# Kernel tuning notes

Measured on AMD Instinct MI355X. Metric: run time of the kernel, lower is better.

The kernel has to match this reference:

```python
import jax, jax.numpy as jnp
import numpy as np


def setup_inputs() -> dict:
    key = jax.random.key(0)
    ks = jax.random.split(key, 5)
    B, S, D = 2, 2048, 1024
    inv = 1.0 / np.sqrt(D)
    inp = {
        "x": jax.random.normal(ks[0], (B, S, D), jnp.float32),
        "Wq": jax.random.normal(ks[1], (D, D), jnp.float32) * inv,
        "bq": jnp.zeros((D,), jnp.float32),
        "Wk": jax.random.normal(ks[2], (D, D), jnp.float32) * inv,
        "bk": jnp.zeros((D,), jnp.float32),
        "Wv": jax.random.normal(ks[3], (D, D), jnp.float32) * inv,
        "bv": jnp.zeros((D,), jnp.float32),
        "Wo": jax.random.normal(ks[4], (D, D), jnp.float32) * inv,
        "bo": jnp.zeros((D,), jnp.float32),
        "num_heads": 16,
        "window_size": 128,
    }
    return inp


def reference(x, Wq, bq, Wk, bk, Wv, bv, Wo, bo, num_heads, window_size):
    B, S, D = x.shape
    H = num_heads
    hd = D // H
    scale = 1.0 / np.sqrt(hd)

    def split_heads(t):  # [B,S,D] -> [B,H,S,hd]
        return t.reshape(B, S, H, hd).transpose(0, 2, 1, 3)

    q = split_heads(x @ Wq + bq)
    k = split_heads(x @ Wk + bk)
    v = split_heads(x @ Wv + bv)

    # dense scores, then sliding-window + causal mask (faithful to original)
    scores = jnp.einsum('bhqd,bhkd->bhqk', q, k) * scale  # [B,H,S,S]
    i = jnp.arange(S)[:, None]
    j = jnp.arange(S)[None, :]
    # position i attends to j in [i - window_size + 1, i]
    mask = (j <= i) & (j > i - window_size)
    scores = jnp.where(mask, scores, -jnp.inf)
    attn_weights = jax.nn.softmax(scores, axis=-1)  # dropout is identity in eval

    out = jnp.einsum('bhqk,bhkd->bhqd', attn_weights, v)  # [B,H,S,hd]
    out = out.transpose(0, 2, 1, 3).reshape(B, S, D)
    return out @ Wo + bo, attn_weights
```

## Files before the change

### kernel.cpp

```cpp
#include <hip/hip_runtime.h>
#include <cmath>

typedef __attribute__((ext_vector_type(8))) __bf16 v8bf;
typedef __attribute__((ext_vector_type(4))) float  v4f;

#define DEV static __device__ __forceinline__

DEV unsigned short f2bf(float f) {
  unsigned u = __builtin_bit_cast(unsigned, f);
  unsigned r = u + 0x7fffu + ((u >> 16) & 1u);
  return (unsigned short)(r >> 16);
}
DEV float bf2f(unsigned short s) {
  return __builtin_bit_cast(float, ((unsigned)s) << 16);
}
DEV v8bf ld8(const unsigned short* p) { return *(const v8bf*)p; }

DEV void gl16(const unsigned short* g, unsigned short* l) {
  __builtin_amdgcn_global_load_lds(
      (const __attribute__((address_space(1))) unsigned int*)g,
      (__attribute__((address_space(3))) unsigned int*)l, 16, 0, 0);
}

DEV void zero_rows(float* __restrict__ wout, int rbase, int wave, int lane) {
  int r0 = rbase + wave * 4;
  for (int rr = 0; rr < 4; rr++) {
    int row = r0 + rr;
    int i = row & 2047;
    int lo = i - 127;
    float* rowp = wout + (size_t)row * 2048;
#pragma unroll
    for (int it = 0; it < 8; it++) {
      int col = it * 256 + lane * 4;
      bool full_in = (col >= lo) && (col + 3 <= i);
      if (full_in) continue;
      bool overlap = (col + 3 >= lo) && (col <= i);
      if (!overlap) {
        v4f z = {0.f, 0.f, 0.f, 0.f};
        __builtin_nontemporal_store(z, (v4f*)(rowp + col));
      } else {
#pragma unroll
        for (int e = 0; e < 4; e++) {
          int j = col + e;
          if (j < lo || j > i) rowp[j] = 0.f;
        }
      }
    }
  }
}

__global__ __launch_bounds__(256) void k_prep(const float* __restrict__ x,
                                              const float* __restrict__ Wq,
                                              const float* __restrict__ Wk,
                                              const float* __restrict__ Wv,
                                              const float* __restrict__ Wo,
                                              const float* __restrict__ bq,
                                              const float* __restrict__ bk,
                                              const float* __restrict__ bv,
                                              unsigned short* __restrict__ xb,
                                              unsigned short* __restrict__ WT,
                                              unsigned short* __restrict__ WoT,
                                              float* __restrict__ bqkv) {
  __shared__ float t[32][33];
  int bx = blockIdx.x, tid = threadIdx.x;
  if (bx < 4096) {
    int i = bx * 256 + tid;
    float4 v = ((const float4*)x)[i];
    unsigned lo = (unsigned)f2bf(v.x) | ((unsigned)f2bf(v.y) << 16);
    unsigned hi = (unsigned)f2bf(v.z) | ((unsigned)f2bf(v.w) << 16);
    ((uint2*)xb)[i] = make_uint2(lo, hi);
  } else if (bx < 8192) {
    int rem = bx - 4096;
    int z = rem >> 10, r2 = rem & 1023;
    const float* src = (z == 0) ? Wq : (z == 1) ? Wk : (z == 2) ? Wv : Wo;
    unsigned short* dst = (z < 3) ? WT + z * 1048576 : WoT;
    int n0 = (r2 & 31) * 32, k0 = (r2 >> 5) * 32;
    int tx = tid & 31, ty = tid >> 5;
    for (int r = ty; r < 32; r += 8)
      t[r][tx] = src[(k0 + r) * 1024 + n0 + tx];
    __syncthreads();
    for (int r = ty; r < 32; r += 8)
      dst[(n0 + r) * 1024 + k0 + tx] = f2bf(t[tx][r]);
  } else {
    int i = (bx - 8192) * 256 + tid;
    float v = (i < 1024) ? bq[i] : (i < 2048 ? bk[i - 1024] : bv[i - 2048]);
    bqkv[i] = v;
  }
}

__global__ __launch_bounds__(256) void k_gemm1(const unsigned short* __restrict__ A,
                                               const unsigned short* __restrict__ Bt,
                                               const float* __restrict__ bias,
                                               unsigned short* __restrict__ QK,
                                               unsigned short* __restrict__ Vtg) {
  constexpr int K = 1024;
  __shared__ __attribute__((aligned(16))) unsigned short As[128 * 32];
  __shared__ __attribute__((aligned(16))) unsigned short Bs[128 * 32];
  int tid = threadIdx.x;
  int wave = tid >> 6, lane = tid & 63;
  int gid = blockIdx.x;
  int n0 = (gid % 24) * 128, m0 = (gid / 24) * 128;
  int wm = (wave >> 1) * 64, wn = (wave & 1) * 64;
  int m = lane & 15, q4 = lane >> 4;
  int arow = tid >> 2, acol = (tid & 3) * 8;
  v4f acc[4][4] = {};
  const unsigned short* ga0 = A + (m0 + arow) * K + acol;
  const unsigned short* ga1 = A + (m0 + 64 + arow) * K + acol;
  const unsigned short* gb0 = Bt + (n0 + arow) * K + acol;
  const unsigned short* gb1 = Bt + (n0 + 64 + arow) * K + acol;
  unsigned short* lA0 = As + wave * 512;
  unsigned short* lA1 = As + 2048 + wave * 512;
  unsigned short* lB0 = Bs + wave * 512;
  unsigned short* lB1 = Bs + 2048 + wave * 512;

  for (int kt = 0; kt < K; kt += 32) {
    gl16(ga0 + kt, lA0);
    gl16(ga1 + kt, lA1);
    gl16(gb0 + kt, lB0);
    gl16(gb1 + kt, lB1);
    __syncthreads();
    v8bf af[4], bfv[4];
#pragma unroll
    for (int mt = 0; mt < 4; mt++) af[mt] = ld8(&As[(wm + mt * 16 + m) * 32 + q4 * 8]);
#pragma unroll
    for (int nt = 0; nt < 4; nt++) bfv[nt] = ld8(&Bs[(wn + nt * 16 + m) * 32 + q4 * 8]);
#pragma unroll
    for (int mt = 0; mt < 4; mt++)
#pragma unroll
      for (int nt = 0; nt < 4; nt++)
        acc[mt][nt] = __builtin_amdgcn_mfma_f32_16x16x32_bf16(af[mt], bfv[nt], acc[mt][nt], 0, 0, 0);
    __syncthreads();
  }
  if (n0 < 2048) {
#pragma unroll
    for (int mt = 0; mt < 4; mt++)
#pragma unroll
      for (int nt = 0; nt < 4; nt++) {
        int col = n0 + wn + nt * 16 + m;
        float bb = bias[col];
#pragma unroll
        for (int r = 0; r < 4; r++) {
          int row = m0 + wm + mt * 16 + q4 * 4 + r;
          QK[row * 2048 + col] = f2bf(acc[mt][nt][r] + bb);
        }
      }
  } else {
    int b = m0 >> 11;
#pragma unroll
    for (int mt = 0; mt < 4; mt++)
#pragma unroll
      for (int nt = 0; nt < 4; nt++) {
        int d = n0 - 2048 + wn + nt * 16 + m;
        int h = d >> 6, dd = d & 63;
        float bb = bias[2048 + d];
        int vrow = (b * 16 + h) * 64 + dd;
        int s0 = (m0 + wm + mt * 16 + q4 * 4) & 2047;
        unsigned short u0 = f2bf(acc[mt][nt][0] + bb);
        unsigned short u1 = f2bf(acc[mt][nt][1] + bb);
        unsigned short u2 = f2bf(acc[mt][nt][2] + bb);
        unsigned short u3 = f2bf(acc[mt][nt][3] + bb);
        unsigned lo = (unsigned)u0 | ((unsigned)u1 << 16);
        unsigned hi = (unsigned)u2 | ((unsigned)u3 << 16);
        *(uint2*)&Vtg[(size_t)vrow * 2048 + s0] = make_uint2(lo, hi);
      }
  }
}

__global__ __launch_bounds__(256) void k_attn(const unsigned short* __restrict__ QK,
                                              const unsigned short* __restrict__ Vtg,
                                              unsigned short* __restrict__ Oatt,
                                              float* __restrict__ wout) {
  constexpr int VTS = 208;
  constexpr int PSS = 168;
  __shared__ __attribute__((aligned(16))) unsigned short Vt[64 * VTS];
  __shared__ __attribute__((aligned(16))) unsigned short Ps[4][16 * PSS];
  int tid = threadIdx.x, wave = tid >> 6, lane = tid & 63;
  int b = blockIdx.z, h = blockIdx.y, i0 = blockIdx.x * 64;
  int kbase = i0 - 128;
  const int ld = 2048;
  const unsigned short* Qg = QK + (size_t)b * 2048 * ld + h * 64;
  const unsigned short* Kg = Qg + 1024;

  const unsigned short* vsrc = Vtg + (size_t)(b * 16 + h) * 64 * 2048;
  for (int idx = tid; idx < 1536; idx += 256) {
    int row = idx / 24, c16 = idx % 24;
    int gcol = kbase + c16 * 8;
    if (gcol < 0) gcol = 0;
    v8bf vv = ld8(vsrc + (size_t)row * 2048 + gcol);
    *(v8bf*)&Vt[row * VTS + c16 * 8] = vv;
  }
  {
    int row = tid >> 2, c4 = (tid & 3) * 4;
    *(uint2*)&Vt[row * VTS + 192 + c4] = make_uint2(0u, 0u);
  }
  for (int c = lane; c < 16 * 24; c += 64)
    Ps[wave][(c / 24) * PSS + 144 + (c % 24)] = 0;
  __syncthreads();

  int qb = i0 + wave * 16;
  int m = lane & 15, q4 = lane >> 4;

  const unsigned short* qrow = Qg + (qb + m) * ld;
  v8bf qa0 = ld8(qrow + q4 * 8);
  v8bf qa1 = ld8(qrow + 32 + q4 * 8);

  v4f sc[9];
#pragma unroll
  for (int n = 0; n < 9; n++) {
    int key = kbase + wave * 16 + n * 16 + m;
    int kg = key < 0 ? 0 : key;
    const unsigned short* krow = Kg + kg * ld;
    v8bf kb0 = ld8(krow + q4 * 8);
    v8bf kb1 = ld8(krow + 32 + q4 * 8);
    v4f z = {0.f, 0.f, 0.f, 0.f};
    z = __builtin_amdgcn_mfma_f32_16x16x32_bf16(qa0, kb0, z, 0, 0, 0);
    z = __builtin_amdgcn_mfma_f32_16x16x32_bf16(qa1, kb1, z, 0, 0, 0);
    sc[n] = z;
  }
  float mx[4] = {-3e38f, -3e38f, -3e38f, -3e38f};
#pragma unroll
  for (int n = 0; n < 9; n++)
#pragma unroll
    for (int r = 0; r < 4; r++) {
      int i = qb + q4 * 4 + r;
      int j = kbase + wave * 16 + n * 16 + m;
      float v = sc[n][r] * 0.125f;
      bool ok = (j >= 0) && (j <= i) && (j > i - 128);
      v = ok ? v : -3e38f;
      sc[n][r] = v;
      mx[r] = fmaxf(mx[r], v);
    }
#pragma unroll
  for (int o = 1; o < 16; o <<= 1)
#pragma unroll
    for (int r = 0; r < 4; r++) mx[r] = fmaxf(mx[r], __shfl_xor(mx[r], o, 64));
  float sum[4] = {0.f, 0.f, 0.f, 0.f};
#pragma unroll
  for (int n = 0; n < 9; n++)
#pragma unroll
    for (int r = 0; r < 4; r++) {
      float p = __expf(sc[n][r] - mx[r]);
      sc[n][r] = p;
      sum[r] += p;
    }
#pragma unroll
  for (int o = 1; o < 16; o <<= 1)
#pragma unroll
    for (int r = 0; r < 4; r++) sum[r] += __shfl_xor(sum[r], o, 64);
  float inv[4];
#pragma unroll
  for (int r = 0; r < 4; r++) inv[r] = 1.0f / sum[r];

#pragma unroll
  for (int n = 0; n < 9; n++)
#pragma unroll
    for (int r = 0; r < 4; r++)
      Ps[wave][(q4 * 4 + r) * PSS + n * 16 + m] = f2bf(sc[n][r] * inv[r]);
  __syncthreads();

  v4f oacc[4] = {};
#pragma unroll
  for (int c = 0; c < 5; c++) {
    v8bf pa = ld8(&Ps[wave][m * PSS + c * 32 + q4 * 8]);
#pragma unroll
    for (int dt = 0; dt < 4; dt++) {
      v8bf vb = ld8(&Vt[(dt * 16 + m) * VTS + wave * 16 + c * 32 + q4 * 8]);
      oacc[dt] = __builtin_amdgcn_mfma_f32_16x16x32_bf16(pa, vb, oacc[dt], 0, 0, 0);
    }
  }
#pragma unroll
  for (int dt = 0; dt < 4; dt++)
#pragma unroll
    for (int r = 0; r < 4; r++)
      Oatt[(b * 2048 + qb + q4 * 4 + r) * 1024 + h * 64 + dt * 16 + m] = f2bf(oacc[dt][r]);

  for (int R = 0; R < 16; R++) {
    int iq = qb + R;
    float* rowp = wout + (size_t)((b * 16 + h) * 2048 + iq) * 2048;
    int lo = iq - 127;
    int t0 = R + 1 + lane * 2;
    float p0 = bf2f(Ps[wave][R * PSS + t0]);
    float p1 = bf2f(Ps[wave][R * PSS + t0 + 1]);
    int j0 = lo + lane * 2;
    if (j0 >= 0) rowp[j0] = p0;
    if (j0 + 1 >= 0) rowp[j0 + 1] = p1;
  }

  int rbase = (b * 16 + h) * 2048 + i0;
#pragma unroll
  for (int k4 = 0; k4 < 4; k4++)
    zero_rows(wout, rbase + k4 * 16, wave, lane);
}

__global__ __launch_bounds__(256) void k_tail(const unsigned short* __restrict__ Oat,
                                              const unsigned short* __restrict__ WoT,
                                              const float* __restrict__ bo,
                                              float* __restrict__ out) {
  __shared__ __attribute__((aligned(16))) unsigned short As[128 * 32];
  __shared__ __attribute__((aligned(16))) unsigned short Bs[128 * 32];
  int tid = threadIdx.x, wave = tid >> 6, lane = tid & 63;
  int bx = blockIdx.x;
  constexpr int K = 1024;
  int n0 = (bx & 7) * 128, m0 = (bx >> 3) * 128;
  int wm = (wave >> 1) * 64, wn = (wave & 1) * 64;
  int m = lane & 15, q4 = lane >> 4;
  int arow = tid >> 2, acol = (tid & 3) * 8;
  v4f acc[4][4] = {};
  const unsigned short* ga0 = Oat + (m0 + arow) * K + acol;
  const unsigned short* ga1 = Oat + (m0 + 64 + arow) * K + acol;
  const unsigned short* gb0 = WoT + (n0 + arow) * K + acol;
  const unsigned short* gb1 = WoT + (n0 + 64 + arow) * K + acol;
  unsigned short* lA0 = As + wave * 512;
  unsigned short* lA1 = As + 2048 + wave * 512;
  unsigned short* lB0 = Bs + wave * 512;
  unsigned short* lB1 = Bs + 2048 + wave * 512;
  for (int kt = 0; kt < K; kt += 32) {
    gl16(ga0 + kt, lA0);
    gl16(ga1 + kt, lA1);
    gl16(gb0 + kt, lB0);
    gl16(gb1 + kt, lB1);
    __syncthreads();
    v8bf af[4], bfv[4];
#pragma unroll
    for (int mt = 0; mt < 4; mt++) af[mt] = ld8(&As[(wm + mt * 16 + m) * 32 + q4 * 8]);
#pragma unroll
    for (int nt = 0; nt < 4; nt++) bfv[nt] = ld8(&Bs[(wn + nt * 16 + m) * 32 + q4 * 8]);
#pragma unroll
    for (int mt = 0; mt < 4; mt++)
#pragma unroll
      for (int nt = 0; nt < 4; nt++)
        acc[mt][nt] = __builtin_amdgcn_mfma_f32_16x16x32_bf16(af[mt], bfv[nt], acc[mt][nt], 0, 0, 0);
    __syncthreads();
  }
#pragma unroll
  for (int mt = 0; mt < 4; mt++)
#pragma unroll
    for (int nt = 0; nt < 4; nt++) {
      int col = n0 + wn + nt * 16 + m;
      float bb = bo[col];
#pragma unroll
      for (int r = 0; r < 4; r++) {
        int row = m0 + wm + mt * 16 + q4 * 4 + r;
        out[row * 1024 + col] = acc[mt][nt][r] + bb;
      }
    }
}

extern "C" void kernel_launch(void* const* d_in, const int* in_sizes, int n_in,
                              void* d_out, int out_size, void* d_ws, size_t ws_size,
                              hipStream_t stream) {
  (void)in_sizes; (void)n_in; (void)out_size; (void)ws_size;
  const float* x  = (const float*)d_in[0];
  const float* Wq = (const float*)d_in[1];
  const float* bq = (const float*)d_in[2];
  const float* Wk = (const float*)d_in[3];
  const float* bk = (const float*)d_in[4];
  const float* Wv = (const float*)d_in[5];
  const float* bv = (const float*)d_in[6];
  const float* Wo = (const float*)d_in[7];
  const float* bo = (const float*)d_in[8];

  char* ws = (char*)d_ws;
  unsigned short* xb   = (unsigned short*)(ws);
  unsigned short* WT   = (unsigned short*)(ws + 8388608);
  unsigned short* WoT  = (unsigned short*)(ws + 14680064);
  float*          bqkv = (float*)(ws + 16777216);
  unsigned short* QK   = (unsigned short*)(ws + 16789504);
  unsigned short* Oat  = (unsigned short*)(ws + 33566720);
  unsigned short* Vtg  = (unsigned short*)(ws + 41955328);

  float* out  = (float*)d_out;
  float* wout = out + 4194304;

  k_prep<<<8204, 256, 0, stream>>>(x, Wq, Wk, Wv, Wo, bq, bk, bv, xb, WT, WoT, bqkv);
  k_gemm1<<<768, 256, 0, stream>>>(xb, WT, bqkv, QK, Vtg);
  k_attn<<<dim3(32, 16, 2), 256, 0, stream>>>(QK, Vtg, Oat, wout);
  k_tail<<<256, 256, 0, stream>>>(Oat, WoT, bo, out);
}
```

Before: 673.8 us.

## Fuse all stages into one cooperative persistent kernel with zero-fill overlap

```diff
diff --git a/kernel.cpp b/kernel.cpp
--- a/kernel.cpp
+++ b/kernel.cpp
@@ -1,5 +1,8 @@
 #include <hip/hip_runtime.h>
+#include <hip/hip_cooperative_groups.h>
 #include <cmath>
+
+namespace cg = cooperative_groups;
 
 typedef __attribute__((ext_vector_type(8))) __bf16 v8bf;
 typedef __attribute__((ext_vector_type(4))) float  v4f;
@@ -49,20 +52,12 @@
   }
 }
 
-__global__ __launch_bounds__(256) void k_prep(const float* __restrict__ x,
-                                              const float* __restrict__ Wq,
-                                              const float* __restrict__ Wk,
-                                              const float* __restrict__ Wv,
-                                              const float* __restrict__ Wo,
-                                              const float* __restrict__ bq,
-                                              const float* __restrict__ bk,
-                                              const float* __restrict__ bv,
-                                              unsigned short* __restrict__ xb,
-                                              unsigned short* __restrict__ WT,
-                                              unsigned short* __restrict__ WoT,
-                                              float* __restrict__ bqkv) {
-  __shared__ float t[32][33];
-  int bx = blockIdx.x, tid = threadIdx.x;
+DEV void prep_unit(int bx, int tid, float* tt,
+                   const float* x, const float* Wq, const float* Wk,
+                   const float* Wv, const float* Wo, const float* bq,
+                   const float* bk, const float* bv,
+                   unsigned short* xb, unsigned short* WT,
+                   unsigned short* WoT, float* bqkv) {
   if (bx < 4096) {
     int i = bx * 256 + tid;
     float4 v = ((const float4*)x)[i];
@@ -77,10 +72,11 @@
     int n0 = (r2 & 31) * 32, k0 = (r2 >> 5) * 32;
     int tx = tid & 31, ty = tid >> 5;
     for (int r = ty; r < 32; r += 8)
-      t[r][tx] = src[(k0 + r) * 1024 + n0 + tx];
+      tt[r * 33 + tx] = src[(k0 + r) * 1024 + n0 + tx];
     __syncthreads();
     for (int r = ty; r < 32; r += 8)
-      dst[(n0 + r) * 1024 + k0 + tx] = f2bf(t[tx][r]);
+      dst[(n0 + r) * 1024 + k0 + tx] = f2bf(tt[tx * 33 + r]);
+    __syncthreads();
   } else {
     int i = (bx - 8192) * 256 + tid;
     float v = (i < 1024) ? bq[i] : (i < 2048 ? bk[i - 1024] : bv[i - 2048]);
@@ -88,17 +84,14 @@
   }
 }
 
-__global__ __launch_bounds__(256) void k_gemm1(const unsigned short* __restrict__ A,
-                                               const unsigned short* __restrict__ Bt,
-                                               const float* __restrict__ bias,
-                                               unsigned short* __restrict__ QK,
-                                               unsigned short* __restrict__ Vtg) {
+DEV void gemm1_tile(int gid, int tid, unsigned short* SM,
+                    const unsigned short* A, const unsigned short* Bt,
+                    const float* bias, unsigned short* QK,
+                    unsigned short* Vtg) {
   constexpr int K = 1024;
-  __shared__ __attribute__((aligned(16))) unsigned short As[128 * 32];
-  __shared__ __attribute__((aligned(16))) unsigned short Bs[128 * 32];
-  int tid = threadIdx.x;
+  unsigned short* As = SM;
+  unsigned short* Bs = SM + 4096;
   int wave = tid >> 6, lane = tid & 63;
-  int gid = blockIdx.x;
   int n0 = (gid % 24) * 128, m0 = (gid / 24) * 128;
   int wm = (wave >> 1) * 64, wn = (wave & 1) * 64;
   int m = lane & 15, q4 = lane >> 4;
@@ -166,16 +159,14 @@
   }
 }
 
-__global__ __launch_bounds__(256) void k_attn(const unsigned short* __restrict__ QK,
-                                              const unsigned short* __restrict__ Vtg,
-                                              unsigned short* __restrict__ Oatt,
-                                              float* __restrict__ wout) {
+DEV void attn_unit(int b, int h, int i0, int tid, unsigned short* SM,
+                   const unsigned short* QK, const unsigned short* Vtg,
+                   unsigned short* Oatt, float* wout) {
   constexpr int VTS = 208;
   constexpr int PSS = 168;
-  __shared__ __attribute__((aligned(16))) unsigned short Vt[64 * VTS];
-  __shared__ __attribute__((aligned(16))) unsigned short Ps[4][16 * PSS];
-  int tid = threadIdx.x, wave = tid >> 6, lane = tid & 63;
-  int b = blockIdx.z, h = blockIdx.y, i0 = blockIdx.x * 64;
+  unsigned short* Vt = SM;
+  int wave = tid >> 6, lane = tid & 63;
+  unsigned short* Psw = SM + 13312 + wave * (16 * PSS);
   int kbase = i0 - 128;
   const int ld = 2048;
   const unsigned short* Qg = QK + (size_t)b * 2048 * ld + h * 64;
@@ -194,7 +185,7 @@
     *(uint2*)&Vt[row * VTS + 192 + c4] = make_uint2(0u, 0u);
   }
   for (int c = lane; c < 16 * 24; c += 64)
-    Ps[wave][(c / 24) * PSS + 144 + (c % 24)] = 0;
+    Psw[(c / 24) * PSS + 144 + (c % 24)] = 0;
   __syncthreads();
 
   int qb = i0 + wave * 16;
@@ -255,13 +246,13 @@
   for (int n = 0; n < 9; n++)
 #pragma unroll
     for (int r = 0; r < 4; r++)
-      Ps[wave][(q4 * 4 + r) * PSS + n * 16 + m] = f2bf(sc[n][r] * inv[r]);
+      Psw[(q4 * 4 + r) * PSS + n * 16 + m] = f2bf(sc[n][r] * inv[r]);
   __syncthreads();
 
   v4f oacc[4] = {};
 #pragma unroll
   for (int c = 0; c < 5; c++) {
-    v8bf pa = ld8(&Ps[wave][m * PSS + c * 32 + q4 * 8]);
+    v8bf pa = ld8(&Psw[m * PSS + c * 32 + q4 * 8]);
 #pragma unroll
     for (int dt = 0; dt < 4; dt++) {
       v8bf vb = ld8(&Vt[(dt * 16 + m) * VTS + wave * 16 + c * 32 + q4 * 8]);
@@ -279,29 +270,22 @@
     float* rowp = wout + (size_t)((b * 16 + h) * 2048 + iq) * 2048;
     int lo = iq - 127;
     int t0 = R + 1 + lane * 2;
-    float p0 = bf2f(Ps[wave][R * PSS + t0]);
-    float p1 = bf2f(Ps[wave][R * PSS + t0 + 1]);
+    float p0 = bf2f(Psw[R * PSS + t0]);
+    float p1 = bf2f(Psw[R * PSS + t0 + 1]);
     int j0 = lo + lane * 2;
     if (j0 >= 0) rowp[j0] = p0;
     if (j0 + 1 >= 0) rowp[j0 + 1] = p1;
   }
-
-  int rbase = (b * 16 + h) * 2048 + i0;
-#pragma unroll
-  for (int k4 = 0; k4 < 4; k4++)
-    zero_rows(wout, rbase + k4 * 16, wave, lane);
-}
-
-__global__ __launch_bounds__(256) void k_tail(const unsigned short* __restrict__ Oat,
-                                              const unsigned short* __restrict__ WoT,
-                                              const float* __restrict__ bo,
-                                              float* __restrict__ out) {
-  __shared__ __attribute__((aligned(16))) unsigned short As[128 * 32];
-  __shared__ __attribute__((aligned(16))) unsigned short Bs[128 * 32];
-  int tid = threadIdx.x, wave = tid >> 6, lane = tid & 63;
-  int bx = blockIdx.x;
+}
+
+DEV void tail_tile(int gid, int tid, unsigned short* SM,
+                   const unsigned short* Oat, const unsigned short* WoT,
+                   const float* bo, float* out) {
   constexpr int K = 1024;
-  int n0 = (bx & 7) * 128, m0 = (bx >> 3) * 128;
+  unsigned short* As = SM;
+  unsigned short* Bs = SM + 4096;
+  int wave = tid >> 6, lane = tid & 63;
+  int n0 = (gid & 7) * 128, m0 = (gid >> 3) * 128;
   int wm = (wave >> 1) * 64, wn = (wave & 1) * 64;
   int m = lane & 15, q4 = lane >> 4;
   int arow = tid >> 2, acol = (tid & 3) * 8;
@@ -346,6 +330,74 @@
     }
 }
 
+__global__ __launch_bounds__(256, 2) void k_mega(
+    const float* __restrict__ x,  const float* __restrict__ Wq,
+    const float* __restrict__ Wk, const float* __restrict__ Wv,
+    const float* __restrict__ Wo, const float* __restrict__ bq,
+    const float* __restrict__ bk, const float* __restrict__ bv,
+    const float* __restrict__ bo,
+    unsigned short* __restrict__ xb,  unsigned short* __restrict__ WT,
+    unsigned short* __restrict__ WoT, float* __restrict__ bqkv,
+    unsigned short* __restrict__ QK,  unsigned short* __restrict__ Vtg,
+    unsigned short* __restrict__ Oat, float* __restrict__ out,
+    float* __restrict__ wout, unsigned* __restrict__ qctr) {
+  cg::grid_group grid = cg::this_grid();
+  __shared__ __attribute__((aligned(16))) unsigned short SM[24064];
+  __shared__ unsigned s_u;
+  int tid = threadIdx.x, wave = tid >> 6, lane = tid & 63;
+  int bid = blockIdx.x, nb = gridDim.x;
+
+  if (bid == 0 && tid < 3) atomicExch(&qctr[tid], 0u);
+  for (int u = bid; u < 8204; u += nb)
+    prep_unit(u, tid, (float*)SM, x, Wq, Wk, Wv, Wo, bq, bk, bv, xb, WT, WoT, bqkv);
+  grid.sync();
+
+  for (;;) {
+    if (tid == 0) s_u = atomicAdd(&qctr[0], 1u);
+    __syncthreads();
+    unsigned u = s_u;
+    __syncthreads();
+    if (u >= 2304u) break;
+    unsigned r = u % 3u, base = u / 3u;
+    if (r == 0) {
+      gemm1_tile((int)base, tid, SM, xb, WT, bqkv, QK, Vtg);
+    } else {
+      int c = (int)(base * 2u + (r - 1u));
+      zero_rows(wout, c * 32, wave, lane);
+      zero_rows(wout, c * 32 + 16, wave, lane);
+    }
+  }
+  grid.sync();
+
+  for (;;) {
+    if (tid == 0) s_u = atomicAdd(&qctr[1], 1u);
+    __syncthreads();
+    unsigned u = s_u;
+    __syncthreads();
+    if (u >= 1536u) break;
+    unsigned r = u % 3u, base = u / 3u;
+    if (r < 2) {
+      int a = (int)(base * 2u + r);
+      int i0 = (a & 31) * 64, h = (a >> 5) & 15, b = a >> 9;
+      attn_unit(b, h, i0, tid, SM, QK, Vtg, Oat, wout);
+    } else {
+      int c = 1536 + (int)base;
+      zero_rows(wout, c * 32, wave, lane);
+      zero_rows(wout, c * 32 + 16, wave, lane);
+    }
+  }
+  grid.sync();
+
+  for (;;) {
+    if (tid == 0) s_u = atomicAdd(&qctr[2], 1u);
+    __syncthreads();
+    unsigned u = s_u;
+    __syncthreads();
+    if (u >= 256u) break;
+    tail_tile((int)u, tid, SM, Oat, WoT, bo, out);
+  }
+}
+
 extern "C" void kernel_launch(void* const* d_in, const int* in_sizes, int n_in,
                               void* d_out, int out_size, void* d_ws, size_t ws_size,
                               hipStream_t stream) {
@@ -368,12 +420,26 @@
   unsigned short* QK   = (unsigned short*)(ws + 16789504);
   unsigned short* Oat  = (unsigned short*)(ws + 33566720);
   unsigned short* Vtg  = (unsigned short*)(ws + 41955328);
+  unsigned*       qctr = (unsigned*)(ws + 50343936);
 
   float* out  = (float*)d_out;
   float* wout = out + 4194304;
 
-  k_prep<<<8204, 256, 0, stream>>>(x, Wq, Wk, Wv, Wo, bq, bk, bv, xb, WT, WoT, bqkv);
-  k_gemm1<<<768, 256, 0, stream>>>(xb, WT, bqkv, QK, Vtg);
-  k_attn<<<dim3(32, 16, 2), 256, 0, stream>>>(QK, Vtg, Oat, wout);
-  k_tail<<<256, 256, 0, stream>>>(Oat, WoT, bo, out);
-}
+  static int occ = 0;
+  if (occ == 0) {
+    int tmp = 0;
+    if (hipOccupancyMaxActiveBlocksPerMultiprocessor(&tmp, k_mega, 256, 0) != hipSuccess || tmp < 1)
+      tmp = 1;
+    occ = tmp;
+  }
+  int nb = occ * 256;
+  if (nb > 768) nb = 768;
+  if (nb < 256) nb = 256;
+
+  void* args[] = {(void*)&x,  (void*)&Wq, (void*)&Wk, (void*)&Wv, (void*)&Wo,
+                  (void*)&bq, (void*)&bk, (void*)&bv, (void*)&bo,
+                  (void*)&xb, (void*)&WT, (void*)&WoT, (void*)&bqkv,
+                  (void*)&QK, (void*)&Vtg, (void*)&Oat, (void*)&out,
+                  (void*)&wout, (void*)&qctr};
+  hipLaunchCooperativeKernel((const void*)k_mega, dim3(nb), dim3(256), args, 0, stream);
+}
```

Result: slower. 827.2 us (+22.8%).
